# Kernel optimization log

Hardware: AMD Instinct MI355X
Metric: run time of the kernel (lower is better)

Reference implementation:

```python
import jax, jax.numpy as jnp
import numpy as np

B, S, HID, NH = 8, 1024, 1024, 16
HD = HID // NH  # head_dim = 64


def setup_inputs() -> dict:
    key = jax.random.key(0)
    ks = jax.random.split(key, 8)
    inp = {
        "key": jax.random.normal(ks[0], (B, S, HID), dtype=jnp.float32),
        "value": jax.random.normal(ks[1], (B, S, HID), dtype=jnp.float32),
        "query": jax.random.normal(ks[2], (B, S, HID), dtype=jnp.float32),
        "attention_mask": jax.random.randint(ks[3], (B, 1, 1, S), 0, 2, dtype=jnp.int32),
        # nn.Linear weights (out, in) with xavier-normal init, zero-ish bias
        "Wk": jax.random.normal(ks[4], (HID, HID), dtype=jnp.float32) * float(np.sqrt(2.0 / (HID + HID))),
        "bk": jax.random.normal(ks[5], (HID,), dtype=jnp.float32) * 0.01,
        "Wv": jax.random.normal(ks[6], (HID, HID), dtype=jnp.float32) * float(np.sqrt(2.0 / (HID + HID))),
        "bv": jax.random.normal(ks[7], (HID,), dtype=jnp.float32) * 0.01,
    }
    return inp


def _split_heads(x):
    # [B,S,HID] -> [B,NH,S,HD]
    return x.reshape(B, S, NH, HD).transpose(0, 2, 1, 3)


def reference(key, value, query, attention_mask, Wk, bk, Wv, bv):
    # NOTE: original torch code projects BOTH query and key with keyProject
    q = _split_heads(query @ Wk.T + bk)
    k = _split_heads(key @ Wk.T + bk)
    v = _split_heads(value @ Wv.T + bv)

    scores = jnp.einsum("bhqd,bhkd->bhqk", q, k) / jnp.sqrt(jnp.float32(HD))

    mask = attention_mask.astype(bool)  # [B,1,1,S] broadcasts over heads/queries
    scores = jnp.where(mask, scores, -jnp.inf)
    probs = jax.nn.softmax(scores, axis=-1)
    probs = jnp.where(mask, probs, 0.0)  # XSoftmax zeroes masked positions

    out = jnp.einsum("bhqk,bhkd->bhqd", probs, v)  # [B,NH,S,HD]
    return out.transpose(0, 2, 1, 3).reshape(B, S, HID)
```

## Files before the change

kernel.cpp:

```cpp
#include <hip/hip_runtime.h>
#include <hip/hip_bf16.h>
#include <stdint.h>

#define B_   8
#define S_   1024
#define HID_ 1024
#define NH_  16
#define HD_  64

typedef __bf16 bf16_t;
typedef __bf16 bf16x8 __attribute__((ext_vector_type(8)));
typedef __bf16 bf16x4 __attribute__((ext_vector_type(4)));
typedef __bf16 bf16x2 __attribute__((ext_vector_type(2)));
typedef float  f32x4  __attribute__((ext_vector_type(4)));
typedef float  f32x16 __attribute__((ext_vector_type(16)));
typedef uint32_t u32x4 __attribute__((ext_vector_type(4)));

#define MFMA16(a,b,c) __builtin_amdgcn_mfma_f32_16x16x32_bf16(a,b,c,0,0,0)
#define MFMA32(a,b,c) __builtin_amdgcn_mfma_f32_32x32x16_bf16(a,b,c,0,0,0)

typedef const __attribute__((address_space(1))) void* as1_t;
typedef __attribute__((address_space(3))) void* as3_t;
#define GLD16(g, s) __builtin_amdgcn_global_load_lds((as1_t)(g), (as3_t)(s), 16, 0, 0)

__device__ __forceinline__ float fexp2(float x) {
#if __has_builtin(__builtin_amdgcn_exp2f)
    return __builtin_amdgcn_exp2f(x);
#else
    return exp2f(x);
#endif
}

__device__ __forceinline__ uint32_t pk2(float a, float b) {
    bf16x2 v; v[0] = (bf16_t)a; v[1] = (bf16_t)b;
    return __builtin_bit_cast(uint32_t, v);
}

__global__ void conv_kernel(const float* __restrict__ src, bf16_t* __restrict__ dst, int n8) {
    int i = blockIdx.x * 256 + threadIdx.x;
    const int stride = gridDim.x * 256;
    for (; i < n8; i += stride) {
        const float4 a = ((const float4*)src)[2 * i];
        const float4 b = ((const float4*)src)[2 * i + 1];
        bf16x8 o;
        o[0] = (bf16_t)a.x; o[1] = (bf16_t)a.y; o[2] = (bf16_t)a.z; o[3] = (bf16_t)a.w;
        o[4] = (bf16_t)b.x; o[5] = (bf16_t)b.y; o[6] = (bf16_t)b.z; o[7] = (bf16_t)b.w;
        ((bf16x8*)dst)[i] = o;
    }
}

__global__ void maskbias_kernel(const int* __restrict__ mask, float* __restrict__ bias, int n) {
    const int i = blockIdx.x * 256 + threadIdx.x;
    if (i < n) bias[i] = mask[i] ? 0.f : -60000.f;
}

template<int Z>
__global__ __launch_bounds__(256) void proj_kernel(
    const bf16_t* __restrict__ A, const bf16_t* __restrict__ W,
    const float* __restrict__ bias, bf16_t* __restrict__ dst)
{
    __shared__ bf16_t Al[128][64];
    __shared__ bf16_t Bl[128][64];

    const int bid = blockIdx.x;
    const int n0  = (bid & 7) * 128;
    const int m0  = (bid >> 3) * 128;

    const int tid = threadIdx.x, w = tid >> 6, lane = tid & 63;
    const int lr = lane & 15, lg = lane >> 4;
    const int wm = (w >> 1) * 64, wn = (w & 1) * 64;
    const int srow = lane >> 3, scol = (lane & 7) * 8;

    f32x4 acc[4][4];
#pragma unroll
    for (int i = 0; i < 4; ++i)
#pragma unroll
        for (int j = 0; j < 4; ++j) acc[i][j] = (f32x4){0.f, 0.f, 0.f, 0.f};

#pragma unroll 1
    for (int kt = 0; kt < 16; ++kt) {
        const int k0 = kt * 64;
#pragma unroll
        for (int j = 0; j < 4; ++j) {
            const int flat = w * 4 + j;
            GLD16(A + (size_t)(m0 + flat * 8 + srow) * 1024 + k0 + scol,
                  (uint8_t*)Al + flat * 1024);
            GLD16(W + (size_t)(n0 + flat * 8 + srow) * 1024 + k0 + scol,
                  (uint8_t*)Bl + flat * 1024);
        }
        __syncthreads();
#pragma unroll
        for (int kk = 0; kk < 2; ++kk) {
            bf16x8 af[4], bfr[4];
#pragma unroll
            for (int i = 0; i < 4; ++i)
                af[i] = *(const bf16x8*)(&Al[wm + i * 16 + lr][kk * 32 + lg * 8]);
#pragma unroll
            for (int j = 0; j < 4; ++j)
                bfr[j] = *(const bf16x8*)(&Bl[wn + j * 16 + lr][kk * 32 + lg * 8]);
#pragma unroll
            for (int i = 0; i < 4; ++i)
#pragma unroll
                for (int j = 0; j < 4; ++j)
                    acc[i][j] = MFMA16(af[i], bfr[j], acc[i][j]);
        }
        __syncthreads();
    }

    const float qscale = 0.18033688011112042f;
#pragma unroll
    for (int j = 0; j < 4; ++j) {
        const int ncol = n0 + wn + j * 16 + lr;
        const float bj = bias[ncol];
#pragma unroll
        for (int i = 0; i < 4; ++i) {
            const int m = m0 + wm + i * 16 + lg * 4;
            f32x4 v = acc[i][j];
            if (Z == 0) {
#pragma unroll
                for (int r = 0; r < 4; ++r)
                    dst[(size_t)(m + r) * 1024 + ncol] = (bf16_t)((v[r] + bj) * qscale);
            } else if (Z == 1) {
#pragma unroll
                for (int r = 0; r < 4; ++r)
                    dst[(size_t)(m + r) * 1024 + ncol] = (bf16_t)(v[r] + bj);
            } else {
                const int h = ncol >> 6, d = ncol & 63;
                const int b = m >> 10, s0 = m & 1023;
                bf16x4 pk;
#pragma unroll
                for (int r = 0; r < 4; ++r) pk[r] = (bf16_t)(v[r] + bj);
                *(bf16x4*)(&dst[((size_t)(b * 16 + h) * 64 + d) * 1024 + s0]) = pk;
            }
        }
    }
}

__global__ __launch_bounds__(256) void attn_kernel(
    const bf16_t* __restrict__ qw, const bf16_t* __restrict__ kw,
    const bf16_t* __restrict__ vt, const float* __restrict__ mb,
    float* __restrict__ out)
{
    const int bid  = blockIdx.x;
    const int xcd  = bid & 7;
    const int slot = bid >> 3;
    const int bh   = xcd * 16 + (slot & 15);
    const int qt   = slot >> 4;
    const int b = bh >> 4, h = bh & 15;
    const int tid = threadIdx.x, w = tid >> 6, lane = tid & 63;
    const int lq = lane & 31, hi = lane >> 5;
    const int q0 = qt * 128 + w * 32;

    const bf16_t* qrow = qw + (size_t)(b * 1024 + q0 + lq) * 1024 + h * 64 + hi * 8;
    bf16x8 qf[4];
#pragma unroll
    for (int c = 0; c < 4; ++c) qf[c] = *(const bf16x8*)(qrow + c * 16);

    const bf16_t* kbase = kw + (size_t)(b * 1024) * 1024 + h * 64 + hi * 8;
    const bf16_t* vbase = vt + ((size_t)bh << 16) + (size_t)lq * 1024 + hi * 8;
    const float*  bb    = mb + b * 1024 + hi * 4;

    f32x16 accO0 = (f32x16)0.f, accO1 = (f32x16)0.f;
    float mrun = -30000.f, lrun = 0.f;

#pragma unroll 1
    for (int t = 0; t < 32; ++t) {
        const int kb = t * 32;
        f32x4 bias4[4];
#pragma unroll
        for (int g = 0; g < 4; ++g) bias4[g] = *(const f32x4*)(bb + kb + g * 8);
        bf16x8 kf[4];
#pragma unroll
        for (int c = 0; c < 4; ++c)
            kf[c] = *(const bf16x8*)(kbase + (size_t)(kb + lq) * 1024 + c * 16);
        const bf16x8 vf00 = *(const bf16x8*)(vbase + kb);
        const bf16x8 vf01 = *(const bf16x8*)(vbase + kb + 16);
        const bf16x8 vf10 = *(const bf16x8*)(vbase + 32 * 1024 + kb);
        const bf16x8 vf11 = *(const bf16x8*)(vbase + 32 * 1024 + kb + 16);

        f32x16 accP;
#pragma unroll
        for (int r = 0; r < 16; ++r) accP[r] = bias4[r >> 2][r & 3];
        __builtin_amdgcn_s_setprio(1);
#pragma unroll
        for (int c = 0; c < 4; ++c) accP = MFMA32(kf[c], qf[c], accP);
        __builtin_amdgcn_s_setprio(0);

        float x0 = fmaxf(accP[0], accP[1]),   x1 = fmaxf(accP[2], accP[3]);
        float x2 = fmaxf(accP[4], accP[5]),   x3 = fmaxf(accP[6], accP[7]);
        float x4 = fmaxf(accP[8], accP[9]),   x5 = fmaxf(accP[10], accP[11]);
        float x6 = fmaxf(accP[12], accP[13]), x7 = fmaxf(accP[14], accP[15]);
        x0 = fmaxf(x0, x1); x2 = fmaxf(x2, x3); x4 = fmaxf(x4, x5); x6 = fmaxf(x6, x7);
        x0 = fmaxf(x0, x2); x4 = fmaxf(x4, x6);
        float tm = fmaxf(x0, x4);
        tm = fmaxf(tm, __shfl_xor(tm, 32));

        if (!__all(tm <= mrun + 8.f)) {
            const float mn  = fmaxf(mrun, tm);
            const float fac = fexp2(mrun - mn);
            mrun = mn;
            lrun *= fac;
#pragma unroll
            for (int r = 0; r < 16; ++r) {
                const float fr = __shfl(fac, (r & 3) + 8 * (r >> 2) + 4 * hi, 64);
                accO0[r] *= fr; accO1[r] *= fr;
            }
        }

#pragma unroll
        for (int r = 0; r < 16; ++r) accP[r] = fexp2(accP[r] - mrun);
        float s0 = accP[0] + accP[1],   s1 = accP[2] + accP[3];
        float s2 = accP[4] + accP[5],   s3 = accP[6] + accP[7];
        float s4 = accP[8] + accP[9],   s5 = accP[10] + accP[11];
        float s6 = accP[12] + accP[13], s7 = accP[14] + accP[15];
        s0 += s1; s2 += s3; s4 += s5; s6 += s7;
        s0 += s2; s4 += s6;
        float ps = s0 + s4;
        ps += __shfl_xor(ps, 32);
        lrun += ps;

        const uint32_t c0 = pk2(accP[0],  accP[1]),  c1 = pk2(accP[2],  accP[3]);
        const uint32_t c2 = pk2(accP[4],  accP[5]),  c3 = pk2(accP[6],  accP[7]);
        const uint32_t c4 = pk2(accP[8],  accP[9]),  c5 = pk2(accP[10], accP[11]);
        const uint32_t c6 = pk2(accP[12], accP[13]), c7 = pk2(accP[14], accP[15]);
        const uint32_t s0u = __shfl_xor(c0, 32), s1u = __shfl_xor(c1, 32);
        const uint32_t s2u = __shfl_xor(c2, 32), s3u = __shfl_xor(c3, 32);
        const uint32_t s4u = __shfl_xor(c4, 32), s5u = __shfl_xor(c5, 32);
        const uint32_t s6u = __shfl_xor(c6, 32), s7u = __shfl_xor(c7, 32);
        const u32x4 A0 = hi ? (u32x4){s2u, s3u, c2, c3} : (u32x4){c0, c1, s0u, s1u};
        const u32x4 A1 = hi ? (u32x4){s6u, s7u, c6, c7} : (u32x4){c4, c5, s4u, s5u};
        const bf16x8 pa0 = __builtin_bit_cast(bf16x8, A0);
        const bf16x8 pa1 = __builtin_bit_cast(bf16x8, A1);

        __builtin_amdgcn_s_setprio(1);
        accO0 = MFMA32(pa0, vf00, accO0);
        accO0 = MFMA32(pa1, vf01, accO0);
        accO1 = MFMA32(pa0, vf10, accO1);
        accO1 = MFMA32(pa1, vf11, accO1);
        __builtin_amdgcn_s_setprio(0);
    }

    const float inv = 1.f / lrun;
    float* ob = out + (size_t)b * 1048576 + h * 64;
#pragma unroll
    for (int r = 0; r < 16; ++r) {
        const int qr = (r & 3) + 8 * (r >> 2) + 4 * hi;
        const float ir = __shfl(inv, qr, 64);
        ob[(size_t)(q0 + qr) * 1024 + lq]      = accO0[r] * ir;
        ob[(size_t)(q0 + qr) * 1024 + 32 + lq] = accO1[r] * ir;
    }
}

extern "C" void kernel_launch(void* const* d_in, const int* in_sizes, int n_in,
                              void* d_out, int out_size, void* d_ws, size_t ws_size,
                              hipStream_t stream) {
    const float* key_in = (const float*)d_in[0];
    const float* val_in = (const float*)d_in[1];
    const float* qry_in = (const float*)d_in[2];
    const int*   mask   = (const int*)d_in[3];
    const float* Wk     = (const float*)d_in[4];
    const float* bk     = (const float*)d_in[5];
    const float* Wv     = (const float*)d_in[6];
    const float* bv     = (const float*)d_in[7];
    float* out = (float*)d_out;

    uint8_t* base = (uint8_t*)d_ws;
    const size_t SZ_IN = (size_t)8192 * 1024 * 2;
    const size_t SZ_W  = (size_t)1024 * 1024 * 2;
    bf16_t* q_ws  = (bf16_t*)(base);
    bf16_t* k_ws  = (bf16_t*)(base + SZ_IN);
    bf16_t* vt_ws = (bf16_t*)(base + 2 * SZ_IN);
    bf16_t* sbuf  = (bf16_t*)(base + 3 * SZ_IN);
    bf16_t* wkbf  = (bf16_t*)(base + 4 * SZ_IN);
    bf16_t* wvbf  = (bf16_t*)(base + 4 * SZ_IN + SZ_W);
    float*  mbias = (float*) (base + 4 * SZ_IN + 2 * SZ_W);

    conv_kernel<<<512, 256, 0, stream>>>(Wk, wkbf, 131072);
    conv_kernel<<<512, 256, 0, stream>>>(Wv, wvbf, 131072);
    maskbias_kernel<<<32, 256, 0, stream>>>(mask, mbias, 8192);

    conv_kernel<<<1024, 256, 0, stream>>>(qry_in, sbuf, 1048576);
    proj_kernel<0><<<512, 256, 0, stream>>>(sbuf, wkbf, bk, q_ws);
    conv_kernel<<<1024, 256, 0, stream>>>(key_in, sbuf, 1048576);
    proj_kernel<1><<<512, 256, 0, stream>>>(sbuf, wkbf, bk, k_ws);
    conv_kernel<<<1024, 256, 0, stream>>>(val_in, sbuf, 1048576);
    proj_kernel<2><<<512, 256, 0, stream>>>(sbuf, wvbf, bv, vt_ws);

    attn_kernel<<<1024, 256, 0, stream>>>(q_ws, k_ws, vt_ws, mbias, out);
}
```

Measured before the change: 411.1 us.

## Double-buffer projection GEMM, merge Q/K projections, prefetch K tiles in attention

The projection GEMMs move to a 32-wide K step with two LDS buffers, so the next tile's global-to-LDS load is issued while the current tile is multiplied. The Q and K projections share one launch of 1024 blocks, with the key input staged in the not-yet-used V workspace. The attention kernel stages the mask bias in shared memory, adds it after the QK MFMAs, and software-pipelines the K fragment loads one tile ahead. These aim to hide memory latency and reduce launch count and idle tails, at the cost of more registers and extra syncs per K step.

```diff
diff --git a/kernel.cpp b/kernel.cpp
--- a/kernel.cpp
+++ b/kernel.cpp
@@ -54,13 +54,99 @@
     if (i < n) bias[i] = mask[i] ? 0.f : -60000.f;
 }
 
-template<int Z>
-__global__ __launch_bounds__(256) void proj_kernel(
+__device__ __forceinline__ void proj_stage(
     const bf16_t* __restrict__ A, const bf16_t* __restrict__ W,
-    const float* __restrict__ bias, bf16_t* __restrict__ dst)
-{
-    __shared__ bf16_t Al[128][64];
-    __shared__ bf16_t Bl[128][64];
+    bf16_t (*Al)[32], bf16_t (*Bl)[32],
+    int m0, int n0, int k0, int w, int lane)
+{
+#pragma unroll
+    for (int j = 0; j < 2; ++j) {
+        const int ia  = w * 2 + j;
+        const int row = ia * 16 + (lane >> 2);
+        const int ce  = (lane & 3) * 8;
+        GLD16(A + (size_t)(m0 + row) * 1024 + k0 + ce, (uint8_t*)Al + ia * 1024);
+        GLD16(W + (size_t)(n0 + row) * 1024 + k0 + ce, (uint8_t*)Bl + ia * 1024);
+    }
+}
+
+__device__ __forceinline__ void proj_mma(
+    const bf16_t (*Al)[32], const bf16_t (*Bl)[32],
+    int wm, int wn, int lr, int lg, f32x4 acc[4][4])
+{
+    bf16x8 af[4], bfr[4];
+#pragma unroll
+    for (int i = 0; i < 4; ++i)
+        af[i] = *(const bf16x8*)(&Al[wm + i * 16 + lr][lg * 8]);
+#pragma unroll
+    for (int j = 0; j < 4; ++j)
+        bfr[j] = *(const bf16x8*)(&Bl[wn + j * 16 + lr][lg * 8]);
+#pragma unroll
+    for (int i = 0; i < 4; ++i)
+#pragma unroll
+        for (int j = 0; j < 4; ++j)
+            acc[i][j] = MFMA16(af[i], bfr[j], acc[i][j]);
+}
+
+__global__ __launch_bounds__(256) void proj01_kernel(
+    const bf16_t* __restrict__ qstage, const bf16_t* __restrict__ kstage,
+    const bf16_t* __restrict__ wk, const float* __restrict__ bk,
+    bf16_t* __restrict__ q_ws, bf16_t* __restrict__ k_ws)
+{
+    __shared__ bf16_t Al[2][128][32];
+    __shared__ bf16_t Bl[2][128][32];
+
+    const int bid  = blockIdx.x;
+    const int n0   = (bid & 7) * 128;
+    const int slot = bid >> 3;
+    const int z    = slot & 1;
+    const int m0   = (slot >> 1) * 128;
+    const bf16_t* A = z ? kstage : qstage;
+    bf16_t* dst     = z ? k_ws : q_ws;
+
+    const int tid = threadIdx.x, w = tid >> 6, lane = tid & 63;
+    const int lr = lane & 15, lg = lane >> 4;
+    const int wm = (w >> 1) * 64, wn = (w & 1) * 64;
+
+    f32x4 acc[4][4];
+#pragma unroll
+    for (int i = 0; i < 4; ++i)
+#pragma unroll
+        for (int j = 0; j < 4; ++j) acc[i][j] = (f32x4){0.f, 0.f, 0.f, 0.f};
+
+    proj_stage(A, wk, Al[0], Bl[0], m0, n0, 0, w, lane);
+    __syncthreads();
+#pragma unroll 1
+    for (int kt = 0; kt < 32; kt += 2) {
+        proj_stage(A, wk, Al[1], Bl[1], m0, n0, (kt + 1) * 32, w, lane);
+        proj_mma(Al[0], Bl[0], wm, wn, lr, lg, acc);
+        __syncthreads();
+        if (kt + 2 < 32) proj_stage(A, wk, Al[0], Bl[0], m0, n0, (kt + 2) * 32, w, lane);
+        proj_mma(Al[1], Bl[1], wm, wn, lr, lg, acc);
+        __syncthreads();
+    }
+
+    const float scale = z ? 1.0f : 0.18033688011112042f;
+#pragma unroll
+    for (int j = 0; j < 4; ++j) {
+        const int ncol = n0 + wn + j * 16 + lr;
+        const float bj = bk[ncol];
+#pragma unroll
+        for (int i = 0; i < 4; ++i) {
+            const int m = m0 + wm + i * 16 + lg * 4;
+            f32x4 v = acc[i][j];
+#pragma unroll
+            for (int r = 0; r < 4; ++r)
+                dst[(size_t)(m + r) * 1024 + ncol] = (bf16_t)((v[r] + bj) * scale);
+        }
+    }
+}
+
+__global__ __launch_bounds__(256) void proj2_kernel(
+    const bf16_t* __restrict__ vstage, const bf16_t* __restrict__ wv,
+    const float* __restrict__ bv, bf16_t* __restrict__ vt_ws)
+{
+    __shared__ bf16_t Al[2][128][32];
+    __shared__ bf16_t Bl[2][128][32];
 
     const int bid = blockIdx.x;
     const int n0  = (bid & 7) * 128;
@@ -69,7 +155,6 @@
     const int tid = threadIdx.x, w = tid >> 6, lane = tid & 63;
     const int lr = lane & 15, lg = lane >> 4;
     const int wm = (w >> 1) * 64, wn = (w & 1) * 64;
-    const int srow = lane >> 3, scol = (lane & 7) * 8;
 
     f32x4 acc[4][4];
 #pragma unroll
@@ -77,61 +162,32 @@
 #pragma unroll
         for (int j = 0; j < 4; ++j) acc[i][j] = (f32x4){0.f, 0.f, 0.f, 0.f};
 
+    proj_stage(vstage, wv, Al[0], Bl[0], m0, n0, 0, w, lane);
+    __syncthreads();
 #pragma unroll 1
-    for (int kt = 0; kt < 16; ++kt) {
-        const int k0 = kt * 64;
-#pragma unroll
-        for (int j = 0; j < 4; ++j) {
-            const int flat = w * 4 + j;
-            GLD16(A + (size_t)(m0 + flat * 8 + srow) * 1024 + k0 + scol,
-                  (uint8_t*)Al + flat * 1024);
-            GLD16(W + (size_t)(n0 + flat * 8 + srow) * 1024 + k0 + scol,
-                  (uint8_t*)Bl + flat * 1024);
-        }
+    for (int kt = 0; kt < 32; kt += 2) {
+        proj_stage(vstage, wv, Al[1], Bl[1], m0, n0, (kt + 1) * 32, w, lane);
+        proj_mma(Al[0], Bl[0], wm, wn, lr, lg, acc);
         __syncthreads();
-#pragma unroll
-        for (int kk = 0; kk < 2; ++kk) {
-            bf16x8 af[4], bfr[4];
-#pragma unroll
-            for (int i = 0; i < 4; ++i)
-                af[i] = *(const bf16x8*)(&Al[wm + i * 16 + lr][kk * 32 + lg * 8]);
-#pragma unroll
-            for (int j = 0; j < 4; ++j)
-                bfr[j] = *(const bf16x8*)(&Bl[wn + j * 16 + lr][kk * 32 + lg * 8]);
-#pragma unroll
-            for (int i = 0; i < 4; ++i)
-#pragma unroll
-                for (int j = 0; j < 4; ++j)
-                    acc[i][j] = MFMA16(af[i], bfr[j], acc[i][j]);
-        }
+        if (kt + 2 < 32) proj_stage(vstage, wv, Al[0], Bl[0], m0, n0, (kt + 2) * 32, w, lane);
+        proj_mma(Al[1], Bl[1], wm, wn, lr, lg, acc);
         __syncthreads();
     }
 
-    const float qscale = 0.18033688011112042f;
 #pragma unroll
     for (int j = 0; j < 4; ++j) {
         const int ncol = n0 + wn + j * 16 + lr;
-        const float bj = bias[ncol];
+        const float bj = bv[ncol];
+        const int h = ncol >> 6, d = ncol & 63;
 #pragma unroll
         for (int i = 0; i < 4; ++i) {
             const int m = m0 + wm + i * 16 + lg * 4;
+            const int b = m >> 10, s0 = m & 1023;
             f32x4 v = acc[i][j];
-            if (Z == 0) {
-#pragma unroll
-                for (int r = 0; r < 4; ++r)
-                    dst[(size_t)(m + r) * 1024 + ncol] = (bf16_t)((v[r] + bj) * qscale);
-            } else if (Z == 1) {
-#pragma unroll
-                for (int r = 0; r < 4; ++r)
-                    dst[(size_t)(m + r) * 1024 + ncol] = (bf16_t)(v[r] + bj);
-            } else {
-                const int h = ncol >> 6, d = ncol & 63;
-                const int b = m >> 10, s0 = m & 1023;
-                bf16x4 pk;
-#pragma unroll
-                for (int r = 0; r < 4; ++r) pk[r] = (bf16_t)(v[r] + bj);
-                *(bf16x4*)(&dst[((size_t)(b * 16 + h) * 64 + d) * 1024 + s0]) = pk;
-            }
+            bf16x4 pk;
+#pragma unroll
+            for (int r = 0; r < 4; ++r) pk[r] = (bf16_t)(v[r] + bj);
+            *(bf16x4*)(&vt_ws[((size_t)(b * 16 + h) * 64 + d) * 1024 + s0]) = pk;
         }
     }
 }
@@ -141,6 +197,8 @@
     const bf16_t* __restrict__ vt, const float* __restrict__ mb,
     float* __restrict__ out)
 {
+    __shared__ float bl[1024];
+
     const int bid  = blockIdx.x;
     const int xcd  = bid & 7;
     const int slot = bid >> 3;
@@ -151,6 +209,9 @@
     const int lq = lane & 31, hi = lane >> 5;
     const int q0 = qt * 128 + w * 32;
 
+    ((f32x4*)bl)[tid] = ((const f32x4*)(mb + (size_t)b * 1024))[tid];
+    __syncthreads();
+
     const bf16_t* qrow = qw + (size_t)(b * 1024 + q0 + lq) * 1024 + h * 64 + hi * 8;
     bf16x8 qf[4];
 #pragma unroll
@@ -158,33 +219,35 @@
 
     const bf16_t* kbase = kw + (size_t)(b * 1024) * 1024 + h * 64 + hi * 8;
     const bf16_t* vbase = vt + ((size_t)bh << 16) + (size_t)lq * 1024 + hi * 8;
-    const float*  bb    = mb + b * 1024 + hi * 4;
 
     f32x16 accO0 = (f32x16)0.f, accO1 = (f32x16)0.f;
     float mrun = -30000.f, lrun = 0.f;
 
-#pragma unroll 1
-    for (int t = 0; t < 32; ++t) {
+    auto LOADK = [&](bf16x8 (&kf)[4], int t) {
         const int kb = t * 32;
-        f32x4 bias4[4];
-#pragma unroll
-        for (int g = 0; g < 4; ++g) bias4[g] = *(const f32x4*)(bb + kb + g * 8);
-        bf16x8 kf[4];
 #pragma unroll
         for (int c = 0; c < 4; ++c)
             kf[c] = *(const bf16x8*)(kbase + (size_t)(kb + lq) * 1024 + c * 16);
+    };
+
+    auto PROCESS = [&](const bf16x8 (&kf)[4], int t) {
+        const int kb = t * 32;
         const bf16x8 vf00 = *(const bf16x8*)(vbase + kb);
         const bf16x8 vf01 = *(const bf16x8*)(vbase + kb + 16);
         const bf16x8 vf10 = *(const bf16x8*)(vbase + 32 * 1024 + kb);
         const bf16x8 vf11 = *(const bf16x8*)(vbase + 32 * 1024 + kb + 16);
-
-        f32x16 accP;
-#pragma unroll
-        for (int r = 0; r < 16; ++r) accP[r] = bias4[r >> 2][r & 3];
+        f32x4 bias4[4];
+#pragma unroll
+        for (int g = 0; g < 4; ++g)
+            bias4[g] = *(const f32x4*)(&bl[kb + g * 8 + hi * 4]);
+
+        f32x16 accP = (f32x16)0.f;
         __builtin_amdgcn_s_setprio(1);
 #pragma unroll
         for (int c = 0; c < 4; ++c) accP = MFMA32(kf[c], qf[c], accP);
         __builtin_amdgcn_s_setprio(0);
+#pragma unroll
+        for (int r = 0; r < 16; ++r) accP[r] += bias4[r >> 2][r & 3];
 
         float x0 = fmaxf(accP[0], accP[1]),   x1 = fmaxf(accP[2], accP[3]);
         float x2 = fmaxf(accP[4], accP[5]),   x3 = fmaxf(accP[6], accP[7]);
@@ -238,6 +301,16 @@
         accO1 = MFMA32(pa0, vf10, accO1);
         accO1 = MFMA32(pa1, vf11, accO1);
         __builtin_amdgcn_s_setprio(0);
+    };
+
+    bf16x8 kfA[4], kfB[4];
+    LOADK(kfA, 0);
+#pragma unroll 1
+    for (int t = 0; t < 32; t += 2) {
+        LOADK(kfB, t + 1);
+        PROCESS(kfA, t);
+        if (t + 2 < 32) LOADK(kfA, t + 2);
+        PROCESS(kfB, t + 1);
     }
 
     const float inv = 1.f / lrun;
@@ -280,11 +353,11 @@
     maskbias_kernel<<<32, 256, 0, stream>>>(mask, mbias, 8192);
 
     conv_kernel<<<1024, 256, 0, stream>>>(qry_in, sbuf, 1048576);
-    proj_kernel<0><<<512, 256, 0, stream>>>(sbuf, wkbf, bk, q_ws);
-    conv_kernel<<<1024, 256, 0, stream>>>(key_in, sbuf, 1048576);
-    proj_kernel<1><<<512, 256, 0, stream>>>(sbuf, wkbf, bk, k_ws);
+    conv_kernel<<<1024, 256, 0, stream>>>(key_in, (bf16_t*)vt_ws, 1048576);
+    proj01_kernel<<<1024, 256, 0, stream>>>(sbuf, (const bf16_t*)vt_ws, wkbf, bk,
+                                            q_ws, k_ws);
     conv_kernel<<<1024, 256, 0, stream>>>(val_in, sbuf, 1048576);
-    proj_kernel<2><<<512, 256, 0, stream>>>(sbuf, wvbf, bv, vt_ws);
+    proj2_kernel<<<512, 256, 0, stream>>>(sbuf, wvbf, bv, vt_ws);
 
     attn_kernel<<<1024, 256, 0, stream>>>(q_ws, k_ws, vt_ws, mbias, out);
 }
```

Result: faster. 372.0 us (-9.5%).
